# Optimization experiments

Hardware: AMD Instinct MI355X
Metric: run time of the kernel (lower is better)

Reference implementation:

```python
import jax, jax.numpy as jnp
import numpy as np

D_MODEL = 1024
N_HEADS = 16
HEAD_DIM = D_MODEL // N_HEADS


def setup_inputs() -> dict:
    key = jax.random.key(0)
    kx, kq, kk, kv, ko = jax.random.split(key, 5)
    scale = 1.0 / np.sqrt(D_MODEL)
    x = jax.random.normal(kx, (4, 2048, D_MODEL), dtype=jnp.float32)
    # nn.Linear weights stored as [out, in]; y = x @ W.T
    W_q = jax.random.normal(kq, (D_MODEL, D_MODEL), dtype=jnp.float32) * scale
    W_k = jax.random.normal(kk, (D_MODEL, D_MODEL), dtype=jnp.float32) * scale
    W_v = jax.random.normal(kv, (D_MODEL, D_MODEL), dtype=jnp.float32) * scale
    W_o = jax.random.normal(ko, (D_MODEL, D_MODEL), dtype=jnp.float32) * scale
    return {"x": x, "W_q": W_q, "W_k": W_k, "W_v": W_v, "W_o": W_o}


def reference(x, W_q, W_k, W_v, W_o):
    B, T, C = x.shape
    H, Dh = N_HEADS, HEAD_DIM

    def proj(W):
        return (x @ W.T).reshape(B, T, H, Dh).transpose(0, 2, 1, 3)  # [B,H,T,Dh]

    Q = proj(W_q)
    K = proj(W_q)  # faithful to source bug: K uses W_q, W_k is unused
    V = proj(W_v)

    scores = jnp.einsum('bhqd,bhkd->bhqk', Q, K) / np.sqrt(Dh)
    causal = jnp.tril(jnp.ones((T, T), dtype=bool))
    scores = jnp.where(causal, scores, -jnp.inf)
    attn = jax.nn.softmax(scores, axis=-1)
    out = jnp.einsum('bhqk,bhkd->bhqd', attn, V)
    out = out.transpose(0, 2, 1, 3).reshape(B, T, C)
    return out @ W_o.T
```

## Files before the change

kernel.cpp:

```cpp
#include <hip/hip_runtime.h>
#include <hip/hip_bf16.h>

typedef unsigned short u16;
typedef __attribute__((ext_vector_type(8))) short bf16x8;
typedef __attribute__((ext_vector_type(4))) float f32x4;

#define B_  4
#define T_  2048
#define C_  1024
#define H_  16
#define DH_ 64
#define M_  (B_*T_)

#define GLDS16(g, l) __builtin_amdgcn_global_load_lds( \
    (const __attribute__((address_space(1))) void*)(g), \
    (__attribute__((address_space(3))) void*)(l), 16, 0, 0)

__device__ __forceinline__ u16 f2b(float f) {
  union { __hip_bfloat16 h; u16 u; } cv;
  cv.h = __float2bfloat16(f);
  return cv.u;
}

__global__ void cast_all_kernel(const float* __restrict__ x,  const float* __restrict__ w0,
                                const float* __restrict__ w1, const float* __restrict__ w2,
                                u16* __restrict__ xo, u16* __restrict__ o0,
                                u16* __restrict__ o1, u16* __restrict__ o2) {
  int bid = blockIdx.x;
  const float* src; u16* dst; int blk;
  if (bid < 8192) { src = x; dst = xo; blk = bid; }
  else {
    int k = bid - 8192, w = k >> 10;
    src = (w == 0) ? w0 : (w == 1) ? w1 : w2;
    dst = (w == 0) ? o0 : (w == 1) ? o1 : o2;
    blk = k & 1023;
  }
  int i = (blk * 256 + threadIdx.x) * 4;
  float4 v = *(const float4*)(src + i);
  unsigned lo = (unsigned)f2b(v.x) | ((unsigned)f2b(v.y) << 16);
  unsigned hi = (unsigned)f2b(v.z) | ((unsigned)f2b(v.w) << 16);
  uint2 p; p.x = lo; p.y = hi;
  *(uint2*)(dst + i) = p;
}

__global__ __launch_bounds__(256) void gemm_bt_kernel(
    const u16* __restrict__ A, const u16* __restrict__ Bm,
    void* __restrict__ Cout, int mode)
{
  constexpr int K = 1024;
  __shared__ __align__(16) u16 As[128 * 64];
  __shared__ __align__(16) u16 Bs[128 * 64];

  const int tid  = threadIdx.x;
  const int wave = tid >> 6, lane = tid & 63;
  const int quad = lane >> 4, l15 = lane & 15;
  const int x7   = l15 & 7;
  const int wm = (wave >> 1) * 64, wn = (wave & 1) * 64;
  const int tm = blockIdx.x * 128, tn = blockIdx.y * 128;

  f32x4 acc[4][4] = {};

  for (int k0 = 0; k0 < K; k0 += 64) {
#pragma unroll
    for (int it = 0; it < 4; it++) {
      int ch  = it * 256 + tid;
      int row = ch >> 3;
      int cc  = (ch & 7) ^ (row & 7);
      GLDS16(A  + (size_t)(tm + row) * K + k0 + cc * 8, &As[(it * 256 + wave * 64) * 8]);
      GLDS16(Bm + (size_t)(tn + row) * K + k0 + cc * 8, &Bs[(it * 256 + wave * 64) * 8]);
    }
    __syncthreads();

#pragma unroll
    for (int ks = 0; ks < 2; ks++) {
      bf16x8 af[4], bfr[4];
#pragma unroll
      for (int t = 0; t < 4; t++) {
        int co = ((ks * 4 + quad) ^ x7) * 8;
        af[t]  = *(const bf16x8*)(&As[(wm + t * 16 + l15) * 64 + co]);
        bfr[t] = *(const bf16x8*)(&Bs[(wn + t * 16 + l15) * 64 + co]);
      }
#pragma unroll
      for (int mt = 0; mt < 4; mt++)
#pragma unroll
        for (int nt = 0; nt < 4; nt++)
          acc[mt][nt] = __builtin_amdgcn_mfma_f32_16x16x32_bf16(af[mt], bfr[nt], acc[mt][nt], 0, 0, 0);
    }
    __syncthreads();
  }

  if (mode == 0) {
    u16* out = (u16*)Cout;
    if (tn < 1024) {
#pragma unroll
      for (int mt = 0; mt < 4; mt++)
#pragma unroll
        for (int nt = 0; nt < 4; nt++)
#pragma unroll
          for (int r = 0; r < 4; r++) {
            int gm = tm + wm + mt * 16 + quad * 4 + r;
            int gn = tn + wn + nt * 16 + l15;
            int b = gm >> 11, t = gm & 2047;
            int h = gn >> 6, d = gn & 63;
            out[((size_t)((b * 16 + h) * 2048 + t) << 6) + d] = f2b(acc[mt][nt][r]);
          }
    } else {
#pragma unroll
      for (int mt = 0; mt < 4; mt++)
#pragma unroll
        for (int nt = 0; nt < 4; nt++) {
          int gm0 = tm + wm + mt * 16 + quad * 4;
          int gn  = tn - 1024 + wn + nt * 16 + l15;
          int b = gm0 >> 11, t0 = gm0 & 2047;
          int h = gn >> 6, d = gn & 63;
          alignas(8) u16 tmp[4];
#pragma unroll
          for (int r = 0; r < 4; r++) tmp[r] = f2b(acc[mt][nt][r]);
          *(ushort4*)(out + 8388608 + (((size_t)(b * 16 + h) * 64 + d) << 11) + t0)
              = *(const ushort4*)tmp;
        }
    }
  } else {
    float* out = (float*)Cout;
#pragma unroll
    for (int mt = 0; mt < 4; mt++)
#pragma unroll
      for (int nt = 0; nt < 4; nt++)
#pragma unroll
        for (int r = 0; r < 4; r++) {
          int gm = tm + wm + mt * 16 + quad * 4 + r;
          int gn = tn + wn + nt * 16 + l15;
          out[(size_t)gm * 1024 + gn] = acc[mt][nt][r];
        }
  }
}

__global__ __launch_bounds__(256, 4) void attn_kernel(
    const u16* __restrict__ Q, const u16* __restrict__ Vt, u16* __restrict__ AO)
{
  constexpr int LDP = 72;
  __shared__ __align__(16) u16 Ks[4096];
  __shared__ __align__(16) u16 Vs[4096];
  __shared__ __align__(16) u16 Ps[4][32 * LDP];

  const int tid  = threadIdx.x;
  const int wave = tid >> 6, lane = tid & 63;
  const int quad = lane >> 4, l15 = lane & 15;
  const int x7   = l15 & 7;
  const int bid  = blockIdx.x;
  const int bh = (bid & 7) * 8 + ((bid >> 3) & 7);
  const int m  = bid >> 6;
  const int i  = (m & 4) ? ((m & 8) ? m - 12 : m + 4) : 15 - m;
  const int b = bh >> 4, h = bh & 15;
  const u16* Qbh = Q  + (size_t)bh * (T_ * DH_);
  const u16* Vbh = Vt + (size_t)bh * (DH_ * T_);
  const int q0w   = i * 128 + wave * 32;
  const int qmaxw = q0w + 31;
  const int nkb   = 2 * i + 2;
  u16* myP = &Ps[wave][0];

  const float C1 = 0.18033688f;
  const float C2 = -28.8539008f;

  bf16x8 qf[2][2];
#pragma unroll
  for (int mt = 0; mt < 2; mt++)
#pragma unroll
    for (int ks = 0; ks < 2; ks++)
      qf[mt][ks] = *(const bf16x8*)(Qbh + (size_t)(q0w + mt * 16 + l15) * DH_ + ks * 32 + quad * 8);

  f32x4 o[2][4] = {};
  float lsum[2][4] = {};

  for (int kb = 0; kb < nkb; kb++) {
    const int k0 = kb * 64;
#pragma unroll
    for (int it = 0; it < 2; it++) {
      int ch  = it * 256 + tid;
      int row = ch >> 3;
      int cc  = (ch & 7) ^ (row & 7);
      GLDS16(Qbh + (size_t)(k0 + row) * DH_ + cc * 8, &Ks[(it * 256 + wave * 64) * 8]);
      GLDS16(Vbh + (size_t)row * T_ + k0 + cc * 8,    &Vs[(it * 256 + wave * 64) * 8]);
    }
    __syncthreads();

    if (k0 <= qmaxw) {
      f32x4 s[2][4] = {};
#pragma unroll
      for (int ks = 0; ks < 2; ks++)
#pragma unroll
        for (int nt = 0; nt < 4; nt++) {
          bf16x8 kf = *(const bf16x8*)(&Ks[(nt * 16 + l15) * 64 + (((ks * 4 + quad) ^ x7) * 8)]);
#pragma unroll
          for (int mt = 0; mt < 2; mt++)
            s[mt][nt] = __builtin_amdgcn_mfma_f32_16x16x32_bf16(qf[mt][ks], kf, s[mt][nt], 0, 0, 0);
        }

      const bool diag = (k0 + 63 > q0w);
#pragma unroll
      for (int mt = 0; mt < 2; mt++)
#pragma unroll
        for (int nt = 0; nt < 4; nt++)
#pragma unroll
          for (int r = 0; r < 4; r++) {
            float p = __builtin_amdgcn_exp2f(s[mt][nt][r] * C1 + C2);
            if (diag) {
              int qg = q0w + mt * 16 + quad * 4 + r;
              int kg = k0 + nt * 16 + l15;
              p = (kg <= qg) ? p : 0.0f;
            }
            lsum[mt][r] += p;
            myP[(mt * 16 + quad * 4 + r) * LDP + nt * 16 + l15] = f2b(p);
          }

#pragma unroll
      for (int ks2 = 0; ks2 < 2; ks2++) {
        bf16x8 pf[2];
#pragma unroll
        for (int mt = 0; mt < 2; mt++)
          pf[mt] = *(const bf16x8*)(&myP[(mt * 16 + l15) * LDP + ks2 * 32 + quad * 8]);
#pragma unroll
        for (int dt = 0; dt < 4; dt++) {
          bf16x8 vf = *(const bf16x8*)(&Vs[(dt * 16 + l15) * 64 + (((ks2 * 4 + quad) ^ x7) * 8)]);
#pragma unroll
          for (int mt = 0; mt < 2; mt++)
            o[mt][dt] = __builtin_amdgcn_mfma_f32_16x16x32_bf16(pf[mt], vf, o[mt][dt], 0, 0, 0);
        }
      }
    }
    __syncthreads();
  }

#pragma unroll
  for (int mt = 0; mt < 2; mt++)
#pragma unroll
    for (int r = 0; r < 4; r++) {
      float v = lsum[mt][r];
#pragma unroll
      for (int off = 1; off < 16; off <<= 1) v += __shfl_xor(v, off, 64);
      float rl = 1.0f / v;
      int t = q0w + mt * 16 + quad * 4 + r;
#pragma unroll
      for (int dt = 0; dt < 4; dt++)
        AO[((size_t)(b * T_ + t)) * C_ + h * DH_ + dt * 16 + l15] = f2b(o[mt][dt][r] * rl);
    }
}

extern "C" void kernel_launch(void* const* d_in, const int* in_sizes, int n_in,
                              void* d_out, int out_size, void* d_ws, size_t ws_size,
                              hipStream_t stream) {
  (void)in_sizes; (void)n_in; (void)out_size; (void)ws_size;
  const float* x  = (const float*)d_in[0];
  const float* Wq = (const float*)d_in[1];
  const float* Wv = (const float*)d_in[3];
  const float* Wo = (const float*)d_in[4];

  u16* Xb  = (u16*)d_ws;
  u16* AOw = Xb;
  u16* Wqb = Xb  + 8388608;
  u16* Wvb = Wqb + 1048576;
  u16* Wob = Wvb + 1048576;
  u16* Qw  = Wob + 1048576;
  u16* Vtw = Qw  + 8388608;

  cast_all_kernel<<<11264, 256, 0, stream>>>(x, Wq, Wv, Wo, Xb, Wqb, Wvb, Wob);

  gemm_bt_kernel<<<dim3(64, 16), 256, 0, stream>>>(Xb, Wqb, (void*)Qw, 0);

  attn_kernel<<<1024, 256, 0, stream>>>(Qw, Vtw, AOw);

  gemm_bt_kernel<<<dim3(64, 8), 256, 0, stream>>>(AOw, Wob, d_out, 1);
}
```

Before: 235.0 us.

## Compute softmax row sums via MFMA, specialize diag tiles, 512-thread output GEMM

The per-element row-sum accumulation and final cross-lane shuffle reduction in attention are replaced by an extra MFMA of the bf16 P tile against a vector of ones. Each lane then holds the full row sum directly. Diagonal and off-diagonal key tiles get compile-time specialized paths, so masking code is dropped from interior tiles. The output projection uses a new 512-thread GEMM kernel with 8 waves per 128x128 tile, which gives more waves and a smaller accumulator per thread. The row sums are now taken from bf16-rounded probabilities rather than fp32, a slight numerical change.

New measurement: 222.5 us. -5.3%, faster.

```diff
diff --git a/kernel.cpp b/kernel.cpp
--- a/kernel.cpp
+++ b/kernel.cpp
@@ -1,5 +1,6 @@
 #include <hip/hip_runtime.h>
 #include <hip/hip_bf16.h>
+#include <type_traits>
 
 typedef unsigned short u16;
 typedef __attribute__((ext_vector_type(8))) short bf16x8;
@@ -135,6 +136,64 @@
   }
 }
 
+__global__ __launch_bounds__(512, 4) void gemm_bt512_kernel(
+    const u16* __restrict__ A, const u16* __restrict__ Bm, float* __restrict__ out)
+{
+  constexpr int K = 1024;
+  __shared__ __align__(16) u16 As[128 * 64];
+  __shared__ __align__(16) u16 Bs[128 * 64];
+
+  const int tid  = threadIdx.x;
+  const int wave = tid >> 6, lane = tid & 63;
+  const int quad = lane >> 4, l15 = lane & 15;
+  const int x7   = l15 & 7;
+  const int wm = (wave >> 1) * 32, wn = (wave & 1) * 64;
+  const int tm = blockIdx.x * 128, tn = blockIdx.y * 128;
+
+  f32x4 acc[2][4] = {};
+
+  for (int k0 = 0; k0 < K; k0 += 64) {
+#pragma unroll
+    for (int it = 0; it < 2; it++) {
+      int ch  = it * 512 + tid;
+      int row = ch >> 3;
+      int cc  = (ch & 7) ^ (row & 7);
+      GLDS16(A  + (size_t)(tm + row) * K + k0 + cc * 8, &As[(it * 512 + wave * 64) * 8]);
+      GLDS16(Bm + (size_t)(tn + row) * K + k0 + cc * 8, &Bs[(it * 512 + wave * 64) * 8]);
+    }
+    __syncthreads();
+
+#pragma unroll
+    for (int ks = 0; ks < 2; ks++) {
+      bf16x8 af[2], bfr[4];
+      int co = ((ks * 4 + quad) ^ x7) * 8;
+#pragma unroll
+      for (int t = 0; t < 2; t++)
+        af[t]  = *(const bf16x8*)(&As[(wm + t * 16 + l15) * 64 + co]);
+#pragma unroll
+      for (int t = 0; t < 4; t++)
+        bfr[t] = *(const bf16x8*)(&Bs[(wn + t * 16 + l15) * 64 + co]);
+#pragma unroll
+      for (int mt = 0; mt < 2; mt++)
+#pragma unroll
+        for (int nt = 0; nt < 4; nt++)
+          acc[mt][nt] = __builtin_amdgcn_mfma_f32_16x16x32_bf16(af[mt], bfr[nt], acc[mt][nt], 0, 0, 0);
+    }
+    __syncthreads();
+  }
+
+#pragma unroll
+  for (int mt = 0; mt < 2; mt++)
+#pragma unroll
+    for (int nt = 0; nt < 4; nt++)
+#pragma unroll
+      for (int r = 0; r < 4; r++) {
+        int gm = tm + wm + mt * 16 + quad * 4 + r;
+        int gn = tn + wn + nt * 16 + l15;
+        out[(size_t)gm * 1024 + gn] = acc[mt][nt][r];
+      }
+}
+
 __global__ __launch_bounds__(256, 4) void attn_kernel(
     const u16* __restrict__ Q, const u16* __restrict__ Vt, u16* __restrict__ AO)
 {
@@ -154,13 +213,14 @@
   const int b = bh >> 4, h = bh & 15;
   const u16* Qbh = Q  + (size_t)bh * (T_ * DH_);
   const u16* Vbh = Vt + (size_t)bh * (DH_ * T_);
-  const int q0w   = i * 128 + wave * 32;
-  const int qmaxw = q0w + 31;
-  const int nkb   = 2 * i + 2;
+  const int q0w = i * 128 + wave * 32;
+  const int kbd = (q0w + 31) >> 6;
+  const int nkb = 2 * i + 2;
   u16* myP = &Ps[wave][0];
 
   const float C1 = 0.18033688f;
   const float C2 = -28.8539008f;
+  const bf16x8 ones = { 0x3F80, 0x3F80, 0x3F80, 0x3F80, 0x3F80, 0x3F80, 0x3F80, 0x3F80 };
 
   bf16x8 qf[2][2];
 #pragma unroll
@@ -170,7 +230,54 @@
       qf[mt][ks] = *(const bf16x8*)(Qbh + (size_t)(q0w + mt * 16 + l15) * DH_ + ks * 32 + quad * 8);
 
   f32x4 o[2][4] = {};
-  float lsum[2][4] = {};
+  f32x4 lsumv[2] = {};
+
+  auto tilecomp = [&](int kb, auto DIAGC) {
+    constexpr bool DIAG = decltype(DIAGC)::value;
+    const int k0 = kb * 64;
+    f32x4 s[2][4] = {};
+#pragma unroll
+    for (int ks = 0; ks < 2; ks++)
+#pragma unroll
+      for (int nt = 0; nt < 4; nt++) {
+        bf16x8 kf = *(const bf16x8*)(&Ks[(nt * 16 + l15) * 64 + (((ks * 4 + quad) ^ x7) * 8)]);
+#pragma unroll
+        for (int mt = 0; mt < 2; mt++)
+          s[mt][nt] = __builtin_amdgcn_mfma_f32_16x16x32_bf16(qf[mt][ks], kf, s[mt][nt], 0, 0, 0);
+      }
+
+#pragma unroll
+    for (int mt = 0; mt < 2; mt++)
+#pragma unroll
+      for (int nt = 0; nt < 4; nt++)
+#pragma unroll
+        for (int r = 0; r < 4; r++) {
+          float p = __builtin_amdgcn_exp2f(s[mt][nt][r] * C1 + C2);
+          if constexpr (DIAG) {
+            int qg = q0w + mt * 16 + quad * 4 + r;
+            int kg = k0 + nt * 16 + l15;
+            p = (kg <= qg) ? p : 0.0f;
+          }
+          myP[(mt * 16 + quad * 4 + r) * LDP + nt * 16 + l15] = f2b(p);
+        }
+
+#pragma unroll
+    for (int ks2 = 0; ks2 < 2; ks2++) {
+      bf16x8 pf[2];
+#pragma unroll
+      for (int mt = 0; mt < 2; mt++) {
+        pf[mt] = *(const bf16x8*)(&myP[(mt * 16 + l15) * LDP + ks2 * 32 + quad * 8]);
+        lsumv[mt] = __builtin_amdgcn_mfma_f32_16x16x32_bf16(pf[mt], ones, lsumv[mt], 0, 0, 0);
+      }
+#pragma unroll
+      for (int dt = 0; dt < 4; dt++) {
+        bf16x8 vf = *(const bf16x8*)(&Vs[(dt * 16 + l15) * 64 + (((ks2 * 4 + quad) ^ x7) * 8)]);
+#pragma unroll
+        for (int mt = 0; mt < 2; mt++)
+          o[mt][dt] = __builtin_amdgcn_mfma_f32_16x16x32_bf16(pf[mt], vf, o[mt][dt], 0, 0, 0);
+      }
+    }
+  };
 
   for (int kb = 0; kb < nkb; kb++) {
     const int k0 = kb * 64;
@@ -184,50 +291,8 @@
     }
     __syncthreads();
 
-    if (k0 <= qmaxw) {
-      f32x4 s[2][4] = {};
-#pragma unroll
-      for (int ks = 0; ks < 2; ks++)
-#pragma unroll
-        for (int nt = 0; nt < 4; nt++) {
-          bf16x8 kf = *(const bf16x8*)(&Ks[(nt * 16 + l15) * 64 + (((ks * 4 + quad) ^ x7) * 8)]);
-#pragma unroll
-          for (int mt = 0; mt < 2; mt++)
-            s[mt][nt] = __builtin_amdgcn_mfma_f32_16x16x32_bf16(qf[mt][ks], kf, s[mt][nt], 0, 0, 0);
-        }
-
-      const bool diag = (k0 + 63 > q0w);
-#pragma unroll
-      for (int mt = 0; mt < 2; mt++)
-#pragma unroll
-        for (int nt = 0; nt < 4; nt++)
-#pragma unroll
-          for (int r = 0; r < 4; r++) {
-            float p = __builtin_amdgcn_exp2f(s[mt][nt][r] * C1 + C2);
-            if (diag) {
-              int qg = q0w + mt * 16 + quad * 4 + r;
-              int kg = k0 + nt * 16 + l15;
-              p = (kg <= qg) ? p : 0.0f;
-            }
-            lsum[mt][r] += p;
-            myP[(mt * 16 + quad * 4 + r) * LDP + nt * 16 + l15] = f2b(p);
-          }
-
-#pragma unroll
-      for (int ks2 = 0; ks2 < 2; ks2++) {
-        bf16x8 pf[2];
-#pragma unroll
-        for (int mt = 0; mt < 2; mt++)
-          pf[mt] = *(const bf16x8*)(&myP[(mt * 16 + l15) * LDP + ks2 * 32 + quad * 8]);
-#pragma unroll
-        for (int dt = 0; dt < 4; dt++) {
-          bf16x8 vf = *(const bf16x8*)(&Vs[(dt * 16 + l15) * 64 + (((ks2 * 4 + quad) ^ x7) * 8)]);
-#pragma unroll
-          for (int mt = 0; mt < 2; mt++)
-            o[mt][dt] = __builtin_amdgcn_mfma_f32_16x16x32_bf16(pf[mt], vf, o[mt][dt], 0, 0, 0);
-        }
-      }
-    }
+    if (kb < kbd)        tilecomp(kb, std::false_type{});
+    else if (kb == kbd)  tilecomp(kb, std::true_type{});
     __syncthreads();
   }
 
@@ -235,10 +300,7 @@
   for (int mt = 0; mt < 2; mt++)
 #pragma unroll
     for (int r = 0; r < 4; r++) {
-      float v = lsum[mt][r];
-#pragma unroll
-      for (int off = 1; off < 16; off <<= 1) v += __shfl_xor(v, off, 64);
-      float rl = 1.0f / v;
+      float rl = 1.0f / lsumv[mt][r];
       int t = q0w + mt * 16 + quad * 4 + r;
 #pragma unroll
       for (int dt = 0; dt < 4; dt++)
@@ -269,5 +331,5 @@
 
   attn_kernel<<<1024, 256, 0, stream>>>(Qw, Vtw, AOw);
 
-  gemm_bt_kernel<<<dim3(64, 8), 256, 0, stream>>>(AOw, Wob, d_out, 1);
-}
+  gemm_bt512_kernel<<<dim3(64, 8), 512, 0, stream>>>(AOw, Wob, (float*)d_out);
+}
```
